# Kernel optimization log

Measured on AMD Instinct MI355X. Metric: run time of the kernel, lower is better.

The kernel has to match this reference:

```python
import jax, jax.numpy as jnp
import numpy as np

# Grids: sparse_shape=(41,320,320); after spcv1 stride(2,1,1) pad1 k3 -> (21,320,320);
# after spcv2 stride(2,1,1) pad(0,1,1) k3 -> (10,320,320); after spcv3 k(3,1,1) stride(2,1,1) -> (4,320,320)
GRID0 = (41, 320, 320)
GRID1 = (21, 320, 320)
GRID2 = (10, 320, 320)
GRID3 = (4, 320, 320)
T = 3
C_IN = 16
BN_EPS = 1e-3


def _idx_grid(coords, shape):
    g = -np.ones(shape, np.int32)
    g[coords[:, 0], coords[:, 1], coords[:, 2]] = np.arange(len(coords), dtype=np.int32)
    return g


def _subm_nbrs(coords, grid):
    M = len(coords)
    nbr = -np.ones((M, 27), np.int32)
    sh = np.array(grid.shape)
    k = 0
    for dz in (-1, 0, 1):
        for dy in (-1, 0, 1):
            for dx in (-1, 0, 1):
                c = coords + np.array([dz, dy, dx])
                ok = np.all((c >= 0) & (c < sh), axis=1)
                nbr[ok, k] = grid[c[ok, 0], c[ok, 1], c[ok, 2]]
                k += 1
    return nbr


def _spconv_pairs(coords_in, grid_in, out_shape, ksz, stride, pad):
    ksz = np.array(ksz); st = np.array(stride); pd = np.array(pad); osh = np.array(out_shape)
    cands = []
    for kz in range(ksz[0]):
        for ky in range(ksz[1]):
            for kx in range(ksz[2]):
                o = coords_in + pd - np.array([kz, ky, kx])
                ok = np.all(o % st == 0, axis=1)
                o = o[ok] // st
                ok2 = np.all((o >= 0) & (o < osh), axis=1)
                cands.append(o[ok2])
    coords_out = np.unique(np.concatenate(cands, 0), axis=0)
    M = len(coords_out); K = int(np.prod(ksz))
    idx = -np.ones((M, K), np.int32)
    sh = np.array(grid_in.shape)
    k = 0
    for kz in range(ksz[0]):
        for ky in range(ksz[1]):
            for kx in range(ksz[2]):
                ci = coords_out * st - pd + np.array([kz, ky, kx])
                ok = np.all((ci >= 0) & (ci < sh), axis=1)
                idx[ok, k] = grid_in[ci[ok, 0], ci[ok, 1], ci[ok, 2]]
                k += 1
    return coords_out.astype(np.int32), idx


def setup_inputs() -> dict:
    rng = np.random.default_rng(0)
    # clustered lidar-like active voxels
    nC, nP = 60, 150
    centers = np.stack([rng.uniform(6, 35, nC), rng.uniform(12, 308, nC), rng.uniform(12, 308, nC)], 1)
    pts = centers[:, None, :] + rng.normal(size=(nC, nP, 3)) * np.array([1.2, 2.0, 2.0])
    pts = np.clip(np.round(pts).astype(np.int64).reshape(-1, 3), 0, np.array(GRID0) - 1)
    coords0 = np.unique(pts, axis=0)
    g0 = _idx_grid(coords0, GRID0)
    nbr0 = _subm_nbrs(coords0, g0)
    coords1, idx1 = _spconv_pairs(coords0, g0, GRID1, (3, 3, 3), (2, 1, 1), (1, 1, 1))
    g1 = _idx_grid(coords1, GRID1)
    nbr1 = _subm_nbrs(coords1, g1)
    coords2, idx2 = _spconv_pairs(coords1, g1, GRID2, (3, 3, 3), (2, 1, 1), (0, 1, 1))
    g2 = _idx_grid(coords2, GRID2)
    nbr2 = _subm_nbrs(coords2, g2)
    coords3, idx3 = _spconv_pairs(coords2, g2, GRID3, (3, 1, 1), (2, 1, 1), (0, 0, 0))

    def w(K, ci, co):
        return jnp.asarray(rng.standard_normal((K, ci, co)) / np.sqrt(K * ci), jnp.float32)

    def bn(n, c):
        g = rng.uniform(0.5, 1.5, (n, c)); b = rng.standard_normal((n, c)) * 0.1
        m = rng.standard_normal((n, c)) * 0.1; v = rng.uniform(0.5, 1.5, (n, c))
        return jnp.asarray(np.stack([g, b, m, v], 1), jnp.float32)  # [n,4,c]

    return dict(
        voxel_features=jnp.asarray(rng.standard_normal((T, len(coords0), C_IN)), jnp.float32),
        w_subm1=w(27, 16, 32), w_subm2=w(27, 32, 32), w_spcv1=w(27, 32, 64),
        w_subm3=w(27, 64, 64), w_subm4=w(27, 64, 64), w_subm5=w(27, 64, 64),
        w_spcv2=w(27, 64, 64), w_subm6=w(27, 64, 64), w_subm7=w(27, 64, 64), w_subm8=w(27, 64, 64),
        w_spcv3=w(3, 64, 64),
        w_ad1=jnp.asarray(rng.standard_normal((64, 64)) / 8.0, jnp.float32),
        w_ad2=jnp.asarray(rng.standard_normal((64, 64)) / 8.0, jnp.float32),
        bn32=bn(2, 32), bn64=bn(9, 64), bn_ad=bn(1, 64)[0],
        nbr0=jnp.asarray(nbr0), idx1=jnp.asarray(idx1), nbr1=jnp.asarray(nbr1),
        idx2=jnp.asarray(idx2), nbr2=jnp.asarray(nbr2), idx3=jnp.asarray(idx3),
        coords3=jnp.asarray(coords3))


def _bn_eval(x, p):
    g, b, m, v = p
    return (x - m) * (g * jax.lax.rsqrt(v + BN_EPS)) + b


def _gconv(f, idx, w):
    # gather-GEMM: idx [M,K] (-1 = missing), f [Min,Ci], w [K,Ci,Co]
    g = jnp.where((idx >= 0)[:, :, None], f[jnp.clip(idx, 0)], 0.0)  # [M,K,Ci]
    return jnp.einsum('mki,kio->mo', g, w)


def reference(voxel_features, w_subm1, w_subm2, w_spcv1, w_subm3, w_subm4, w_subm5,
              w_spcv2, w_subm6, w_subm7, w_subm8, w_spcv3, w_ad1, w_ad2,
              bn32, bn64, bn_ad, nbr0, idx1, nbr1, idx2, nbr2, idx3, coords3):
    relu = jax.nn.relu
    s0 = s1 = s2 = None  # cached previous-frame sparse features per level
    outs = []
    for t in range(voxel_features.shape[0]):
        a0 = 0.0 if s0 is None else jnp.mean(s0, 0)
        a1 = 0.0 if s1 is None else jnp.mean(s1, 0)
        a2 = 0.0 if s2 is None else jnp.mean(s2, 0)
        x = relu(_bn_eval(_gconv(voxel_features[t], nbr0, w_subm1), bn32[0]))
        x = relu(_bn_eval(_gconv(x, nbr0, w_subm2), bn32[1]))
        x3 = relu(_bn_eval(_gconv(x, idx1, w_spcv1) + a0, bn64[0])); s0 = x3
        x = relu(_bn_eval(_gconv(x3, nbr1, w_subm3), bn64[1]))
        x = relu(_bn_eval(_gconv(x, nbr1, w_subm4), bn64[2]))
        x6 = relu(_bn_eval(_gconv(x, nbr1, w_subm5), bn64[3]))
        x7 = relu(_bn_eval(_gconv(x6, idx2, w_spcv2) + a1, bn64[4])); s1 = x7
        x = relu(_bn_eval(_gconv(x7, nbr2, w_subm6), bn64[5]))
        x = relu(_bn_eval(_gconv(x, nbr2, w_subm7), bn64[6]))
        x10 = relu(_bn_eval(_gconv(x, nbr2, w_subm8), bn64[7]))
        x11 = relu(_bn_eval(_gconv(x10, idx3, w_spcv3) + a2, bn64[8])); s2 = x11
        dense = jnp.zeros(GRID3 + (64,), x11.dtype).at[coords3[:, 0], coords3[:, 1], coords3[:, 2]].set(x11)
        outs.append(dense.transpose(3, 0, 1, 2).reshape(1, 64 * GRID3[0], GRID3[1], GRID3[2]))
        adapt = lambda s: (relu(_bn_eval(s @ w_ad1, bn_ad)) @ w_ad2) / 10.0
        s0, s1, s2 = adapt(s0), adapt(s1), adapt(s2)
    return jnp.stack(outs)
```

## Files before the change

kernel.cpp:

```cpp
#include <hip/hip_runtime.h>


typedef _Float16 f16;
typedef _Float16 f16x8 __attribute__((ext_vector_type(8)));
typedef float    f32x4 __attribute__((ext_vector_type(4)));

#define BN_EPS_F 1e-3f

__global__ __launch_bounds__(256)
void fill_zero(float4* __restrict__ p, long n4)
{
    long i  = blockIdx.x * 256L + threadIdx.x;
    long st = (long)gridDim.x * 256L;
    float4 z = make_float4(0.f, 0.f, 0.f, 0.f);
    for (; i < n4; i += st) p[i] = z;
}

__global__ __launch_bounds__(256)
void vf_convert(const float* __restrict__ vf, f16* __restrict__ vf16, int nrows)
{
    int i = blockIdx.x * 256 + threadIdx.x;
    if (i >= nrows * 32) return;
    int r = i >> 5, c = i & 31;
    vf16[i] = (c < 16) ? (f16)vf[r * 16 + c] : (f16)0;
}

struct WXA { const float* s; f16* d; int K, Ci, Co, CiD, off; };
struct WXAll { WXA w[11]; };

__global__ __launch_bounds__(256)
void wxform_all(WXAll wa, int total)
{
    int i = blockIdx.x * 256 + threadIdx.x;
    if (i >= total) return;
    int j = 0;
    #pragma unroll
    for (int t = 1; t < 11; ++t) if (i >= wa.w[t].off) j = t;
    const float* s = wa.w[j].s;
    f16* d = wa.w[j].d;
    int Ci = wa.w[j].Ci, Co = wa.w[j].Co, CiD = wa.w[j].CiD;
    int e = i - wa.w[j].off;
    int cc = Co * CiD;
    int k = e / cc; int rem = e - k * cc;
    int co = rem / CiD; int ci = rem - co * CiD;
    float v = (ci < Ci) ? s[((size_t)k * Ci + ci) * Co + co] : 0.f;
    d[e] = (f16)v;
}

template<int Ci, int Co, int K, bool SCATTER>
__global__ __launch_bounds__(256)
void gconv(const f16* __restrict__ fin, const int* __restrict__ idx,
           const f16* __restrict__ wT,
           const float* __restrict__ bnp,
           const float* __restrict__ avec,
           f16* __restrict__ fout,
           const int* __restrict__ coords, float* __restrict__ dout,
           int M, int blocksPerFrame, long finStride, long foutStride)
{
    constexpr int NF  = Co / 16;
    constexpr int KK  = Ci / 32;
    constexpr int CiP = Ci + 8;
    constexpr int cpr = Ci / 8;
    constexpr int CH  = Co * cpr;
    constexpr int NLD = (CH + 255) / 256;

    __shared__ f16 Bw[2][Co * CiP];
    __shared__ int sIdx[64][K];

    const int tid  = threadIdx.x;
    const int lane = tid & 63;
    const int wq   = tid >> 6;
    const int l15  = lane & 15;
    const int kg   = lane >> 4;

    const int bid   = blockIdx.x;
    const int frame = bid / blocksPerFrame;
    const int fb    = bid - frame * blocksPerFrame;
    const f16* finF = fin + (long)frame * finStride;
    f16* foutF      = fout + (long)frame * foutStride;
    const int m0    = fb * 64;

    for (int i = tid; i < 64 * K; i += 256) {
        int r = i / K, k = i - r * K;
        int m = m0 + r;
        sIdx[r][k] = (m < M) ? idx[(long)m * K + k] : -1;
    }
    for (int i = tid; i < CH; i += 256) {
        int co = i / cpr, q = i - co * cpr;
        *(uint4*)&Bw[0][co * CiP + q * 8] = *(const uint4*)&wT[(long)co * Ci + q * 8];
    }
    __syncthreads();

    const int arow = wq * 16 + l15;

    f16x8 afc[KK];
    {
        int n = sIdx[arow][0];
        #pragma unroll
        for (int kk = 0; kk < KK; ++kk) {
            f16x8 v = {};
            if (n >= 0) v = *(const f16x8*)&finF[(long)n * Ci + kk * 32 + kg * 8];
            afc[kk] = v;
        }
    }

    f32x4 acc[NF];
    #pragma unroll
    for (int nf = 0; nf < NF; ++nf) acc[nf] = (f32x4){0.f, 0.f, 0.f, 0.f};

    #pragma unroll 1
    for (int k = 0; k < K; ++k) {
        const bool more = (k + 1 < K);
        uint4 wreg[NLD];
        if (more) {
            #pragma unroll
            for (int u = 0; u < NLD; ++u) {
                int i = tid + u * 256;
                if (i < CH) {
                    int co = i / cpr, q = i - co * cpr;
                    wreg[u] = *(const uint4*)&wT[((long)(k + 1) * Co + co) * Ci + q * 8];
                }
            }
        }
        f16x8 afn[KK];
        {
            int n = more ? sIdx[arow][k + 1] : -1;
            #pragma unroll
            for (int kk = 0; kk < KK; ++kk) {
                f16x8 v = {};
                if (n >= 0) v = *(const f16x8*)&finF[(long)n * Ci + kk * 32 + kg * 8];
                afn[kk] = v;
            }
        }
        const f16* bwb = &Bw[k & 1][0];
        #pragma unroll
        for (int kk = 0; kk < KK; ++kk) {
            #pragma unroll
            for (int nf = 0; nf < NF; ++nf) {
                f16x8 bf = *(const f16x8*)&bwb[(nf * 16 + l15) * CiP + kk * 32 + kg * 8];
                acc[nf] = __builtin_amdgcn_mfma_f32_16x16x32_f16(afc[kk], bf, acc[nf], 0, 0, 0);
            }
        }
        if (more) {
            #pragma unroll
            for (int u = 0; u < NLD; ++u) {
                int i = tid + u * 256;
                if (i < CH) {
                    int co = i / cpr, q = i - co * cpr;
                    *(uint4*)&Bw[(k + 1) & 1][co * CiP + q * 8] = wreg[u];
                }
            }
            __syncthreads();
        }
        #pragma unroll
        for (int kk = 0; kk < KK; ++kk) afc[kk] = afn[kk];
    }

    #pragma unroll
    for (int nf = 0; nf < NF; ++nf) {
        int c = nf * 16 + l15;
        float gg = bnp[c], bb = bnp[Co + c], mu = bnp[2 * Co + c], vv = bnp[3 * Co + c];
        float sc = gg * rsqrtf(vv + BN_EPS_F);
        float sh = bb - mu * sc;
        float av = avec ? avec[c] : 0.f;
        #pragma unroll
        for (int j = 0; j < 4; ++j) {
            int m = m0 + wq * 16 + kg * 4 + j;
            if (m < M) {
                float x = acc[nf][j] + av;
                float y = fmaxf(fmaf(x, sc, sh), 0.f);
                foutF[(long)m * Co + c] = (f16)y;
                if (SCATTER) {
                    int z  = coords[m * 3 + 0];
                    int yy = coords[m * 3 + 1];
                    int xx = coords[m * 3 + 2];
                    dout[(long)(c * 4 + z) * (320 * 320) + yy * 320 + xx] = y;
                }
            }
        }
    }
}

__global__ __launch_bounds__(64)
void adapt_partial3(const f16* __restrict__ x3, const f16* __restrict__ x7,
                    const f16* __restrict__ x11,
                    const float* __restrict__ w_ad1, const float* __restrict__ bn_ad,
                    float* __restrict__ pb,
                    int M1, int M2, int M3, int g1, int g2)
{
    __shared__ float wl[64 * 64];
    const int c = threadIdx.x;
    for (int i = c; i < 64 * 64; i += 64) wl[i] = w_ad1[i];
    float gg = bn_ad[c], bb = bn_ad[64 + c], mu = bn_ad[128 + c], vv = bn_ad[192 + c];
    float sc = gg * rsqrtf(vv + BN_EPS_F);
    float sh = bb - mu * sc;
    __syncthreads();

    int b = blockIdx.x;
    const f16* s; int M, r0;
    if (b < g1)           { s = x3;  M = M1; r0 = b * 64; }
    else if (b < g1 + g2) { s = x7;  M = M2; r0 = (b - g1) * 64; }
    else                  { s = x11; M = M3; r0 = (b - g1 - g2) * 64; }

    float hacc = 0.f;
    int r1 = min(r0 + 64, M);
    for (int r = r0; r < r1; ++r) {
        float acc = 0.f;
        #pragma unroll
        for (int i8 = 0; i8 < 8; ++i8) {
            f16x8 sv = *(const f16x8*)&s[(size_t)r * 64 + i8 * 8];
            #pragma unroll
            for (int e = 0; e < 8; ++e)
                acc = fmaf((float)sv[e], wl[(i8 * 8 + e) * 64 + c], acc);
        }
        hacc += fmaxf(fmaf(acc, sc, sh), 0.f);
    }
    pb[(size_t)b * 64 + c] = hacc;
}

__global__ __launch_bounds__(192)
void adapt_final3(const float* __restrict__ pb, const float* __restrict__ w_ad2,
                  float* __restrict__ av, int g1, int g2, int g3,
                  float invM1, float invM2, float invM3)
{
    __shared__ float h[3][64];
    const int lvl = threadIdx.x >> 6;
    const int c   = threadIdx.x & 63;
    int base = (lvl == 0) ? 0 : (lvl == 1 ? g1 : g1 + g2);
    int n    = (lvl == 0) ? g1 : (lvl == 1 ? g2 : g3);
    float invM = (lvl == 0) ? invM1 : (lvl == 1 ? invM2 : invM3);
    float acc = 0.f;
    for (int i = 0; i < n; ++i) acc += pb[(size_t)(base + i) * 64 + c];
    h[lvl][c] = acc * invM;
    __syncthreads();
    float o = 0.f;
    #pragma unroll 8
    for (int j = 0; j < 64; ++j) o = fmaf(h[lvl][j], w_ad2[j * 64 + c], o);
    av[lvl * 64 + c] = o * 0.1f;
}

extern "C" void kernel_launch(void* const* d_in, const int* in_sizes, int n_in,
                              void* d_out, int out_size, void* d_ws, size_t ws_size,
                              hipStream_t stream)
{
    const float* vf      = (const float*)d_in[0];
    const float* w_subm1 = (const float*)d_in[1];
    const float* w_subm2 = (const float*)d_in[2];
    const float* w_spcv1 = (const float*)d_in[3];
    const float* w_subm3 = (const float*)d_in[4];
    const float* w_subm4 = (const float*)d_in[5];
    const float* w_subm5 = (const float*)d_in[6];
    const float* w_spcv2 = (const float*)d_in[7];
    const float* w_subm6 = (const float*)d_in[8];
    const float* w_subm7 = (const float*)d_in[9];
    const float* w_subm8 = (const float*)d_in[10];
    const float* w_spcv3 = (const float*)d_in[11];
    const float* w_ad1   = (const float*)d_in[12];
    const float* w_ad2   = (const float*)d_in[13];
    const float* bn32    = (const float*)d_in[14];
    const float* bn64    = (const float*)d_in[15];
    const float* bn_ad   = (const float*)d_in[16];
    const int* nbr0    = (const int*)d_in[17];
    const int* idx1    = (const int*)d_in[18];
    const int* nbr1    = (const int*)d_in[19];
    const int* idx2    = (const int*)d_in[20];
    const int* nbr2    = (const int*)d_in[21];
    const int* idx3    = (const int*)d_in[22];
    const int* coords3 = (const int*)d_in[23];

    const int M0 = in_sizes[0]  / (3 * 16);
    const int M1 = in_sizes[18] / 27;
    const int M2 = in_sizes[20] / 27;
    const int M3 = in_sizes[22] / 3;

    char* base = (char*)d_ws;
    size_t off = 0;
    auto alloc = [&](size_t bytes) -> void* {
        void* p = base + off;
        off = (off + bytes + 255) & ~(size_t)255;
        return p;
    };
    f16* wt1  = (f16*)alloc((size_t)27 * 32 * 32 * 2);
    f16* wt2  = (f16*)alloc((size_t)27 * 32 * 32 * 2);
    f16* wtc1 = (f16*)alloc((size_t)27 * 64 * 32 * 2);
    f16* wt3  = (f16*)alloc((size_t)27 * 64 * 64 * 2);
    f16* wt4  = (f16*)alloc((size_t)27 * 64 * 64 * 2);
    f16* wt5  = (f16*)alloc((size_t)27 * 64 * 64 * 2);
    f16* wtc2 = (f16*)alloc((size_t)27 * 64 * 64 * 2);
    f16* wt6  = (f16*)alloc((size_t)27 * 64 * 64 * 2);
    f16* wt7  = (f16*)alloc((size_t)27 * 64 * 64 * 2);
    f16* wt8  = (f16*)alloc((size_t)27 * 64 * 64 * 2);
    f16* wtc3 = (f16*)alloc((size_t)3  * 64 * 64 * 2);
    f16* vf16  = (f16*)alloc((size_t)3 * M0 * 32 * 2);
    f16* buf0a = (f16*)alloc((size_t)3 * M0 * 32 * 2);
    f16* buf0b = (f16*)alloc((size_t)3 * M0 * 32 * 2);
    f16* x3    = (f16*)alloc((size_t)M1 * 64 * 2);
    f16* buf1a = (f16*)alloc((size_t)M1 * 64 * 2);
    f16* buf1b = (f16*)alloc((size_t)M1 * 64 * 2);
    f16* x7    = (f16*)alloc((size_t)M2 * 64 * 2);
    f16* buf2a = (f16*)alloc((size_t)M2 * 64 * 2);
    f16* buf2b = (f16*)alloc((size_t)M2 * 64 * 2);
    f16* x11   = (f16*)alloc((size_t)M3 * 64 * 2);
    float* av  = (float*)alloc(192 * 4);
    const int g1a = (M1 + 63) / 64, g2a = (M2 + 63) / 64, g3a = (M3 + 63) / 64;
    float* pb  = (float*)alloc((size_t)(g1a + g2a + g3a) * 64 * 4);
    (void)ws_size; (void)n_in;

    WXAll wa;
    int woff = 0;
    auto addw = [&](int slot, const float* s, f16* d, int K, int Ci, int Co, int CiD) {
        wa.w[slot] = {s, d, K, Ci, Co, CiD, woff};
        woff += K * Co * CiD;
    };
    addw(0,  w_subm1, wt1,  27, 16, 32, 32);
    addw(1,  w_subm2, wt2,  27, 32, 32, 32);
    addw(2,  w_spcv1, wtc1, 27, 32, 64, 32);
    addw(3,  w_subm3, wt3,  27, 64, 64, 64);
    addw(4,  w_subm4, wt4,  27, 64, 64, 64);
    addw(5,  w_subm5, wt5,  27, 64, 64, 64);
    addw(6,  w_spcv2, wtc2, 27, 64, 64, 64);
    addw(7,  w_subm6, wt6,  27, 64, 64, 64);
    addw(8,  w_subm7, wt7,  27, 64, 64, 64);
    addw(9,  w_subm8, wt8,  27, 64, 64, 64);
    addw(10, w_spcv3, wtc3, 3,  64, 64, 64);
    wxform_all<<<(woff + 255) / 256, 256, 0, stream>>>(wa, woff);
    vf_convert<<<(3 * M0 * 32 + 255) / 256, 256, 0, stream>>>(vf, vf16, 3 * M0);
    fill_zero<<<2048, 256, 0, stream>>>((float4*)d_out, (long)out_size / 4);

    const int g0 = (M0 + 63) / 64;
    const int g1 = (M1 + 63) / 64;
    const int g2 = (M2 + 63) / 64;
    const int g3 = (M3 + 63) / 64;
    const long s0 = (long)M0 * 32;

    gconv<32,32,27,false><<<3 * g0, 256, 0, stream>>>(
        vf16,  nbr0, wt1, bn32,       nullptr, buf0a, nullptr, nullptr, M0, g0, s0, s0);
    gconv<32,32,27,false><<<3 * g0, 256, 0, stream>>>(
        buf0a, nbr0, wt2, bn32 + 128, nullptr, buf0b, nullptr, nullptr, M0, g0, s0, s0);

    for (int t = 0; t < 3; ++t) {
        const float* a0 = (t == 0) ? nullptr : av + 0;
        const float* a1 = (t == 0) ? nullptr : av + 64;
        const float* a2 = (t == 0) ? nullptr : av + 128;
        float* doutT = (float*)d_out + (size_t)t * 256 * 320 * 320;

        gconv<32,64,27,false><<<g1, 256, 0, stream>>>(
            buf0b + (long)t * s0, idx1, wtc1, bn64, a0, x3, nullptr, nullptr, M1, g1, 0, 0);
        gconv<64,64,27,false><<<g1, 256, 0, stream>>>(
            x3,    nbr1, wt3, bn64 + 256,  nullptr, buf1a, nullptr, nullptr, M1, g1, 0, 0);
        gconv<64,64,27,false><<<g1, 256, 0, stream>>>(
            buf1a, nbr1, wt4, bn64 + 512,  nullptr, buf1b, nullptr, nullptr, M1, g1, 0, 0);
        gconv<64,64,27,false><<<g1, 256, 0, stream>>>(
            buf1b, nbr1, wt5, bn64 + 768,  nullptr, buf1a, nullptr, nullptr, M1, g1, 0, 0);
        gconv<64,64,27,false><<<g2, 256, 0, stream>>>(
            buf1a, idx2, wtc2, bn64 + 1024, a1,     x7,    nullptr, nullptr, M2, g2, 0, 0);
        gconv<64,64,27,false><<<g2, 256, 0, stream>>>(
            x7,    nbr2, wt6, bn64 + 1280, nullptr, buf2a, nullptr, nullptr, M2, g2, 0, 0);
        gconv<64,64,27,false><<<g2, 256, 0, stream>>>(
            buf2a, nbr2, wt7, bn64 + 1536, nullptr, buf2b, nullptr, nullptr, M2, g2, 0, 0);
        gconv<64,64,27,false><<<g2, 256, 0, stream>>>(
            buf2b, nbr2, wt8, bn64 + 1792, nullptr, buf2a, nullptr, nullptr, M2, g2, 0, 0);
        gconv<64,64,3,true><<<g3, 256, 0, stream>>>(
            buf2a, idx3, wtc3, bn64 + 2048, a2,    x11,   coords3, doutT,   M3, g3, 0, 0);

        if (t < 2) {
            adapt_partial3<<<g1a + g2a + g3a, 64, 0, stream>>>(
                x3, x7, x11, w_ad1, bn_ad, pb, M1, M2, M3, g1a, g2a);
            adapt_final3<<<1, 192, 0, stream>>>(
                pb, w_ad2, av, g1a, g2a, g3a, 1.f / M1, 1.f / M2, 1.f / M3);
        }
    }
}
```

Baseline: 1.532 ms.

## Fuse all layers into one persistent cooperative kernel with grid syncs

Replaces the chain of about 30 separate launches (weight transform, conversion, zero fill, each conv layer, adapt reductions) with a single cooperative persistent kernel that runs every stage in turn, separated by grid-wide syncs. Conv tiles grow to 128 rows with 512-thread blocks and are walked in a grid-stride loop. The adapt reduction now uses atomicAdd into per-level accumulators instead of per-block partials plus a separate final kernel. Launch overhead and inter-kernel gaps are removed, but grid.sync costs, a fixed grid size, atomic ordering nondeterminism and lower occupancy per block are added.

```diff
diff --git a/kernel.cpp b/kernel.cpp
--- a/kernel.cpp
+++ b/kernel.cpp
@@ -1,71 +1,47 @@
 #include <hip/hip_runtime.h>
-
+#include <hip/hip_cooperative_groups.h>
+
+
+namespace cg = cooperative_groups;
 
 typedef _Float16 f16;
 typedef _Float16 f16x8 __attribute__((ext_vector_type(8)));
 typedef float    f32x4 __attribute__((ext_vector_type(4)));
 
 #define BN_EPS_F 1e-3f
-
-__global__ __launch_bounds__(256)
-void fill_zero(float4* __restrict__ p, long n4)
-{
-    long i  = blockIdx.x * 256L + threadIdx.x;
-    long st = (long)gridDim.x * 256L;
-    float4 z = make_float4(0.f, 0.f, 0.f, 0.f);
-    for (; i < n4; i += st) p[i] = z;
-}
-
-__global__ __launch_bounds__(256)
-void vf_convert(const float* __restrict__ vf, f16* __restrict__ vf16, int nrows)
-{
-    int i = blockIdx.x * 256 + threadIdx.x;
-    if (i >= nrows * 32) return;
-    int r = i >> 5, c = i & 31;
-    vf16[i] = (c < 16) ? (f16)vf[r * 16 + c] : (f16)0;
-}
-
-struct WXA { const float* s; f16* d; int K, Ci, Co, CiD, off; };
-struct WXAll { WXA w[11]; };
-
-__global__ __launch_bounds__(256)
-void wxform_all(WXAll wa, int total)
-{
-    int i = blockIdx.x * 256 + threadIdx.x;
-    if (i >= total) return;
-    int j = 0;
-    #pragma unroll
-    for (int t = 1; t < 11; ++t) if (i >= wa.w[t].off) j = t;
-    const float* s = wa.w[j].s;
-    f16* d = wa.w[j].d;
-    int Ci = wa.w[j].Ci, Co = wa.w[j].Co, CiD = wa.w[j].CiD;
-    int e = i - wa.w[j].off;
-    int cc = Co * CiD;
-    int k = e / cc; int rem = e - k * cc;
-    int co = rem / CiD; int ci = rem - co * CiD;
-    float v = (ci < Ci) ? s[((size_t)k * Ci + ci) * Co + co] : 0.f;
-    d[e] = (f16)v;
-}
+#define SMEM_BYTES 33024
+
+struct WXA { const float* s; int K, Ci, Co, CiD, off; };
+
+struct Args {
+    const float *vf, *w_ad1, *w_ad2, *bn32, *bn64, *bn_ad;
+    const int *nbr0, *idx1, *nbr1, *idx2, *nbr2, *idx3, *coords3;
+    float* dout; long out_n4;
+    f16* wt[11];
+    f16 *vf16, *b0a, *b0b, *x3, *b1a, *b1b, *x7, *b2a, *b2b, *x11;
+    float *hs0, *hs1, *av0, *av1;
+    WXA wx[11]; int wtotal;
+    int M0, M1, M2, M3;
+};
 
 template<int Ci, int Co, int K, bool SCATTER>
-__global__ __launch_bounds__(256)
-void gconv(const f16* __restrict__ fin, const int* __restrict__ idx,
-           const f16* __restrict__ wT,
-           const float* __restrict__ bnp,
-           const float* __restrict__ avec,
-           f16* __restrict__ fout,
-           const int* __restrict__ coords, float* __restrict__ dout,
-           int M, int blocksPerFrame, long finStride, long foutStride)
+__device__ void conv_layer(char* smem,
+    const f16* __restrict__ fin, const int* __restrict__ idx,
+    const f16* __restrict__ wT,
+    const float* __restrict__ bnp, const float* __restrict__ avec,
+    f16* __restrict__ fout,
+    const int* __restrict__ coords, float* __restrict__ dout,
+    int M, int nframes, long finStride, long foutStride)
 {
     constexpr int NF  = Co / 16;
     constexpr int KK  = Ci / 32;
     constexpr int CiP = Ci + 8;
     constexpr int cpr = Ci / 8;
     constexpr int CH  = Co * cpr;
-    constexpr int NLD = (CH + 255) / 256;
-
-    __shared__ f16 Bw[2][Co * CiP];
-    __shared__ int sIdx[64][K];
+    constexpr int NLD = (CH + 511) / 512;
+
+    int (*sIdx)[K] = (int(*)[K])smem;
+    f16* Bw = (f16*)(smem + 13824);
 
     const int tid  = threadIdx.x;
     const int lane = tid & 63;
@@ -73,205 +49,305 @@
     const int l15  = lane & 15;
     const int kg   = lane >> 4;
 
-    const int bid   = blockIdx.x;
-    const int frame = bid / blocksPerFrame;
-    const int fb    = bid - frame * blocksPerFrame;
-    const f16* finF = fin + (long)frame * finStride;
-    f16* foutF      = fout + (long)frame * foutStride;
-    const int m0    = fb * 64;
-
-    for (int i = tid; i < 64 * K; i += 256) {
-        int r = i / K, k = i - r * K;
-        int m = m0 + r;
-        sIdx[r][k] = (m < M) ? idx[(long)m * K + k] : -1;
-    }
-    for (int i = tid; i < CH; i += 256) {
-        int co = i / cpr, q = i - co * cpr;
-        *(uint4*)&Bw[0][co * CiP + q * 8] = *(const uint4*)&wT[(long)co * Ci + q * 8];
-    }
-    __syncthreads();
-
-    const int arow = wq * 16 + l15;
-
-    f16x8 afc[KK];
-    {
-        int n = sIdx[arow][0];
-        #pragma unroll
-        for (int kk = 0; kk < KK; ++kk) {
-            f16x8 v = {};
-            if (n >= 0) v = *(const f16x8*)&finF[(long)n * Ci + kk * 32 + kg * 8];
-            afc[kk] = v;
-        }
-    }
-
-    f32x4 acc[NF];
-    #pragma unroll
-    for (int nf = 0; nf < NF; ++nf) acc[nf] = (f32x4){0.f, 0.f, 0.f, 0.f};
-
-    #pragma unroll 1
-    for (int k = 0; k < K; ++k) {
-        const bool more = (k + 1 < K);
-        uint4 wreg[NLD];
-        if (more) {
-            #pragma unroll
-            for (int u = 0; u < NLD; ++u) {
-                int i = tid + u * 256;
-                if (i < CH) {
-                    int co = i / cpr, q = i - co * cpr;
-                    wreg[u] = *(const uint4*)&wT[((long)(k + 1) * Co + co) * Ci + q * 8];
-                }
-            }
-        }
-        f16x8 afn[KK];
+    const int tpf    = (M + 127) >> 7;
+    const int ntiles = tpf * nframes;
+
+    for (int tile = blockIdx.x; tile < ntiles; tile += gridDim.x) {
+        const int frame = tile / tpf;
+        const int fb    = tile - frame * tpf;
+        const f16* finF = fin + (long)frame * finStride;
+        f16* foutF      = fout + (long)frame * foutStride;
+        const int m0    = fb << 7;
+
+        __syncthreads();
+        for (int i = tid; i < 128 * K; i += 512) {
+            int r = i / K, k = i - r * K;
+            int m = m0 + r;
+            sIdx[r][k] = (m < M) ? idx[(long)m * K + k] : -1;
+        }
+        for (int i = tid; i < CH; i += 512) {
+            int co = i / cpr, q = i - co * cpr;
+            *(uint4*)&Bw[co * CiP + q * 8] = *(const uint4*)&wT[(long)co * Ci + q * 8];
+        }
+        __syncthreads();
+
+        const int arow = wq * 16 + l15;
+
+        f16x8 afc[KK];
         {
-            int n = more ? sIdx[arow][k + 1] : -1;
+            int n = sIdx[arow][0];
             #pragma unroll
             for (int kk = 0; kk < KK; ++kk) {
                 f16x8 v = {};
                 if (n >= 0) v = *(const f16x8*)&finF[(long)n * Ci + kk * 32 + kg * 8];
-                afn[kk] = v;
-            }
-        }
-        const f16* bwb = &Bw[k & 1][0];
+                afc[kk] = v;
+            }
+        }
+
+        f32x4 acc[NF];
         #pragma unroll
-        for (int kk = 0; kk < KK; ++kk) {
-            #pragma unroll
-            for (int nf = 0; nf < NF; ++nf) {
-                f16x8 bf = *(const f16x8*)&bwb[(nf * 16 + l15) * CiP + kk * 32 + kg * 8];
-                acc[nf] = __builtin_amdgcn_mfma_f32_16x16x32_f16(afc[kk], bf, acc[nf], 0, 0, 0);
-            }
-        }
-        if (more) {
-            #pragma unroll
-            for (int u = 0; u < NLD; ++u) {
-                int i = tid + u * 256;
-                if (i < CH) {
-                    int co = i / cpr, q = i - co * cpr;
-                    *(uint4*)&Bw[(k + 1) & 1][co * CiP + q * 8] = wreg[u];
-                }
-            }
-            __syncthreads();
-        }
+        for (int nf = 0; nf < NF; ++nf) acc[nf] = (f32x4){0.f, 0.f, 0.f, 0.f};
+
+        #pragma unroll 1
+        for (int k = 0; k < K; ++k) {
+            const bool more = (k + 1 < K);
+            uint4 wreg[NLD];
+            if (more) {
+                #pragma unroll
+                for (int u = 0; u < NLD; ++u) {
+                    int i = tid + u * 512;
+                    if (i < CH) {
+                        int co = i / cpr, q = i - co * cpr;
+                        wreg[u] = *(const uint4*)&wT[((long)(k + 1) * Co + co) * Ci + q * 8];
+                    }
+                }
+            }
+            f16x8 afn[KK];
+            {
+                int n = more ? sIdx[arow][k + 1] : -1;
+                #pragma unroll
+                for (int kk = 0; kk < KK; ++kk) {
+                    f16x8 v = {};
+                    if (n >= 0) v = *(const f16x8*)&finF[(long)n * Ci + kk * 32 + kg * 8];
+                    afn[kk] = v;
+                }
+            }
+            const f16* bwb = &Bw[(k & 1) * (Co * CiP)];
+            #pragma unroll
+            for (int kk = 0; kk < KK; ++kk)
+                #pragma unroll
+                for (int nf = 0; nf < NF; ++nf) {
+                    f16x8 bf = *(const f16x8*)&bwb[(nf * 16 + l15) * CiP + kk * 32 + kg * 8];
+                    acc[nf] = __builtin_amdgcn_mfma_f32_16x16x32_f16(afc[kk], bf, acc[nf], 0, 0, 0);
+                }
+            if (more) {
+                #pragma unroll
+                for (int u = 0; u < NLD; ++u) {
+                    int i = tid + u * 512;
+                    if (i < CH) {
+                        int co = i / cpr, q = i - co * cpr;
+                        *(uint4*)&Bw[((k + 1) & 1) * (Co * CiP) + co * CiP + q * 8] = wreg[u];
+                    }
+                }
+                __syncthreads();
+            }
+            #pragma unroll
+            for (int kk = 0; kk < KK; ++kk) afc[kk] = afn[kk];
+        }
+
         #pragma unroll
-        for (int kk = 0; kk < KK; ++kk) afc[kk] = afn[kk];
-    }
-
-    #pragma unroll
-    for (int nf = 0; nf < NF; ++nf) {
-        int c = nf * 16 + l15;
-        float gg = bnp[c], bb = bnp[Co + c], mu = bnp[2 * Co + c], vv = bnp[3 * Co + c];
-        float sc = gg * rsqrtf(vv + BN_EPS_F);
-        float sh = bb - mu * sc;
-        float av = avec ? avec[c] : 0.f;
-        #pragma unroll
-        for (int j = 0; j < 4; ++j) {
-            int m = m0 + wq * 16 + kg * 4 + j;
-            if (m < M) {
-                float x = acc[nf][j] + av;
-                float y = fmaxf(fmaf(x, sc, sh), 0.f);
-                foutF[(long)m * Co + c] = (f16)y;
-                if (SCATTER) {
-                    int z  = coords[m * 3 + 0];
-                    int yy = coords[m * 3 + 1];
-                    int xx = coords[m * 3 + 2];
-                    dout[(long)(c * 4 + z) * (320 * 320) + yy * 320 + xx] = y;
-                }
-            }
-        }
-    }
-}
-
-__global__ __launch_bounds__(64)
-void adapt_partial3(const f16* __restrict__ x3, const f16* __restrict__ x7,
-                    const f16* __restrict__ x11,
-                    const float* __restrict__ w_ad1, const float* __restrict__ bn_ad,
-                    float* __restrict__ pb,
-                    int M1, int M2, int M3, int g1, int g2)
-{
-    __shared__ float wl[64 * 64];
-    const int c = threadIdx.x;
-    for (int i = c; i < 64 * 64; i += 64) wl[i] = w_ad1[i];
+        for (int nf = 0; nf < NF; ++nf) {
+            int c = nf * 16 + l15;
+            float gg = bnp[c], bb = bnp[Co + c], mu = bnp[2 * Co + c], vv = bnp[3 * Co + c];
+            float sc = gg * rsqrtf(vv + BN_EPS_F);
+            float sh = bb - mu * sc;
+            float av = avec ? avec[c] : 0.f;
+            #pragma unroll
+            for (int j = 0; j < 4; ++j) {
+                int m = m0 + wq * 16 + kg * 4 + j;
+                if (m < M) {
+                    float x = acc[nf][j] + av;
+                    float y = fmaxf(fmaf(x, sc, sh), 0.f);
+                    foutF[(long)m * Co + c] = (f16)y;
+                    if (SCATTER) {
+                        int z  = coords[m * 3 + 0];
+                        int yy = coords[m * 3 + 1];
+                        int xx = coords[m * 3 + 2];
+                        dout[(long)(c * 4 + z) * (320 * 320) + yy * 320 + xx] = y;
+                    }
+                }
+            }
+        }
+    }
+}
+
+__device__ void adapt_partial(char* smem,
+    const f16* __restrict__ x3, const f16* __restrict__ x7,
+    const f16* __restrict__ x11, int M1, int M2, int M3,
+    const float* __restrict__ w_ad1, const float* __restrict__ bn_ad,
+    float* __restrict__ hs)
+{
+    float* wl = (float*)smem;
+    const int tid = threadIdx.x;
+    __syncthreads();
+    for (int i = tid; i < 64 * 64; i += 512) wl[i] = w_ad1[i];
+    __syncthreads();
+
+    const int sub = tid >> 6;
+    const int c   = tid & 63;
     float gg = bn_ad[c], bb = bn_ad[64 + c], mu = bn_ad[128 + c], vv = bn_ad[192 + c];
     float sc = gg * rsqrtf(vv + BN_EPS_F);
     float sh = bb - mu * sc;
+
+    const int c1 = (M1 + 63) >> 6, c2 = (M2 + 63) >> 6, c3 = (M3 + 63) >> 6;
+    const int ct = c1 + c2 + c3;
+
+    for (int ch = blockIdx.x * 8 + sub; ch < ct; ch += gridDim.x * 8) {
+        const f16* s; int M, r0, lvl;
+        if (ch < c1)           { s = x3;  M = M1; r0 = ch << 6;            lvl = 0; }
+        else if (ch < c1 + c2) { s = x7;  M = M2; r0 = (ch - c1) << 6;     lvl = 1; }
+        else                   { s = x11; M = M3; r0 = (ch - c1 - c2) << 6; lvl = 2; }
+        float hacc = 0.f;
+        int r1 = min(r0 + 64, M);
+        for (int r = r0; r < r1; ++r) {
+            float acc = 0.f;
+            #pragma unroll
+            for (int i8 = 0; i8 < 8; ++i8) {
+                f16x8 sv = *(const f16x8*)&s[(long)r * 64 + i8 * 8];
+                #pragma unroll
+                for (int e = 0; e < 8; ++e)
+                    acc = fmaf((float)sv[e], wl[(i8 * 8 + e) * 64 + c], acc);
+            }
+            hacc += fmaxf(fmaf(acc, sc, sh), 0.f);
+        }
+        atomicAdd(&hs[lvl * 64 + c], hacc);
+    }
+}
+
+__device__ void adapt_final(char* smem,
+    const float* __restrict__ hs, const float* __restrict__ w_ad2,
+    float* __restrict__ av, float invM1, float invM2, float invM3)
+{
+    float* h = (float*)(smem + 16384);
+    const int tid = threadIdx.x;
+    if (tid < 192) {
+        int lvl = tid >> 6;
+        float invM = (lvl == 0) ? invM1 : (lvl == 1 ? invM2 : invM3);
+        h[tid] = hs[tid] * invM;
+    }
     __syncthreads();
-
-    int b = blockIdx.x;
-    const f16* s; int M, r0;
-    if (b < g1)           { s = x3;  M = M1; r0 = b * 64; }
-    else if (b < g1 + g2) { s = x7;  M = M2; r0 = (b - g1) * 64; }
-    else                  { s = x11; M = M3; r0 = (b - g1 - g2) * 64; }
-
-    float hacc = 0.f;
-    int r1 = min(r0 + 64, M);
-    for (int r = r0; r < r1; ++r) {
-        float acc = 0.f;
-        #pragma unroll
-        for (int i8 = 0; i8 < 8; ++i8) {
-            f16x8 sv = *(const f16x8*)&s[(size_t)r * 64 + i8 * 8];
-            #pragma unroll
-            for (int e = 0; e < 8; ++e)
-                acc = fmaf((float)sv[e], wl[(i8 * 8 + e) * 64 + c], acc);
-        }
-        hacc += fmaxf(fmaf(acc, sc, sh), 0.f);
-    }
-    pb[(size_t)b * 64 + c] = hacc;
-}
-
-__global__ __launch_bounds__(192)
-void adapt_final3(const float* __restrict__ pb, const float* __restrict__ w_ad2,
-                  float* __restrict__ av, int g1, int g2, int g3,
-                  float invM1, float invM2, float invM3)
-{
-    __shared__ float h[3][64];
-    const int lvl = threadIdx.x >> 6;
-    const int c   = threadIdx.x & 63;
-    int base = (lvl == 0) ? 0 : (lvl == 1 ? g1 : g1 + g2);
-    int n    = (lvl == 0) ? g1 : (lvl == 1 ? g2 : g3);
-    float invM = (lvl == 0) ? invM1 : (lvl == 1 ? invM2 : invM3);
-    float acc = 0.f;
-    for (int i = 0; i < n; ++i) acc += pb[(size_t)(base + i) * 64 + c];
-    h[lvl][c] = acc * invM;
+    if (tid < 192) {
+        int lvl = tid >> 6, c = tid & 63;
+        float o = 0.f;
+        #pragma unroll 8
+        for (int j = 0; j < 64; ++j) o = fmaf(h[lvl * 64 + j], w_ad2[j * 64 + c], o);
+        av[tid] = o * 0.1f;
+    }
     __syncthreads();
-    float o = 0.f;
-    #pragma unroll 8
-    for (int j = 0; j < 64; ++j) o = fmaf(h[lvl][j], w_ad2[j * 64 + c], o);
-    av[lvl * 64 + c] = o * 0.1f;
+}
+
+__global__ __launch_bounds__(512, 2)
+void mega(Args a)
+{
+    cg::grid_group gg = cg::this_grid();
+    __shared__ __align__(16) char smem[SMEM_BYTES];
+    const int tid  = threadIdx.x;
+    const long gsz = (long)gridDim.x * 512;
+    const long gt  = (long)blockIdx.x * 512 + tid;
+
+    {
+        float4* o4 = (float4*)a.dout;
+        float4 z = make_float4(0.f, 0.f, 0.f, 0.f);
+        for (long i = gt; i < a.out_n4; i += gsz) o4[i] = z;
+        for (int i = (int)gt; i < a.wtotal; i += (int)gsz) {
+            int j = 0;
+            #pragma unroll
+            for (int t = 1; t < 11; ++t) if (i >= a.wx[t].off) j = t;
+            const WXA& W = a.wx[j];
+            int e = i - W.off;
+            int cc = W.Co * W.CiD;
+            int k = e / cc; int rem = e - k * cc;
+            int co = rem / W.CiD; int ci = rem - co * W.CiD;
+            float v = (ci < W.Ci) ? W.s[((long)k * W.Ci + ci) * W.Co + co] : 0.f;
+            a.wt[j][e] = (f16)v;
+        }
+        int nvf = 3 * a.M0 * 32;
+        for (int i = (int)gt; i < nvf; i += (int)gsz) {
+            int r = i >> 5, c = i & 31;
+            a.vf16[i] = (c < 16) ? (f16)a.vf[r * 16 + c] : (f16)0;
+        }
+        if (gt < 192) a.hs0[gt] = 0.f;
+        else if (gt < 384) a.hs1[gt - 192] = 0.f;
+    }
+    gg.sync();
+
+    const long s0 = (long)a.M0 * 32;
+
+    conv_layer<32,32,27,false>(smem, a.vf16, a.nbr0, a.wt[0], a.bn32, nullptr,
+                               a.b0a, nullptr, nullptr, a.M0, 3, s0, s0);
+    gg.sync();
+    conv_layer<32,32,27,false>(smem, a.b0a, a.nbr0, a.wt[1], a.bn32 + 128, nullptr,
+                               a.b0b, nullptr, nullptr, a.M0, 3, s0, s0);
+    gg.sync();
+
+    for (int t = 0; t < 3; ++t) {
+        const float* av = (t == 0) ? nullptr : (t == 1 ? a.av0 : a.av1);
+        float* doutT = a.dout + (long)t * 256 * 320 * 320;
+
+        conv_layer<32,64,27,false>(smem, a.b0b + (long)t * s0, a.idx1, a.wt[2],
+                                   a.bn64, av ? av + 0 : nullptr,
+                                   a.x3, nullptr, nullptr, a.M1, 1, 0, 0);
+        gg.sync();
+        conv_layer<64,64,27,false>(smem, a.x3, a.nbr1, a.wt[3], a.bn64 + 256, nullptr,
+                                   a.b1a, nullptr, nullptr, a.M1, 1, 0, 0);
+        gg.sync();
+        conv_layer<64,64,27,false>(smem, a.b1a, a.nbr1, a.wt[4], a.bn64 + 512, nullptr,
+                                   a.b1b, nullptr, nullptr, a.M1, 1, 0, 0);
+        gg.sync();
+        conv_layer<64,64,27,false>(smem, a.b1b, a.nbr1, a.wt[5], a.bn64 + 768, nullptr,
+                                   a.b1a, nullptr, nullptr, a.M1, 1, 0, 0);
+        gg.sync();
+        conv_layer<64,64,27,false>(smem, a.b1a, a.idx2, a.wt[6], a.bn64 + 1024,
+                                   av ? av + 64 : nullptr,
+                                   a.x7, nullptr, nullptr, a.M2, 1, 0, 0);
+        gg.sync();
+        conv_layer<64,64,27,false>(smem, a.x7, a.nbr2, a.wt[7], a.bn64 + 1280, nullptr,
+                                   a.b2a, nullptr, nullptr, a.M2, 1, 0, 0);
+        gg.sync();
+        conv_layer<64,64,27,false>(smem, a.b2a, a.nbr2, a.wt[8], a.bn64 + 1536, nullptr,
+                                   a.b2b, nullptr, nullptr, a.M2, 1, 0, 0);
+        gg.sync();
+        conv_layer<64,64,27,false>(smem, a.b2b, a.nbr2, a.wt[9], a.bn64 + 1792, nullptr,
+                                   a.b2a, nullptr, nullptr, a.M2, 1, 0, 0);
+        gg.sync();
+        conv_layer<64,64,3,true>(smem, a.b2a, a.idx3, a.wt[10], a.bn64 + 2048,
+                                 av ? av + 128 : nullptr,
+                                 a.x11, a.coords3, doutT, a.M3, 1, 0, 0);
+        gg.sync();
+
+        if (t < 2) {
+            float* hs = (t == 0) ? a.hs0 : a.hs1;
+            adapt_partial(smem, a.x3, a.x7, a.x11, a.M1, a.M2, a.M3,
+                          a.w_ad1, a.bn_ad, hs);
+            gg.sync();
+            if (blockIdx.x == 0)
+                adapt_final(smem, hs, a.w_ad2, (t == 0) ? a.av0 : a.av1,
+                            1.f / a.M1, 1.f / a.M2, 1.f / a.M3);
+            gg.sync();
+        }
+    }
 }
 
 extern "C" void kernel_launch(void* const* d_in, const int* in_sizes, int n_in,
                               void* d_out, int out_size, void* d_ws, size_t ws_size,
                               hipStream_t stream)
 {
-    const float* vf      = (const float*)d_in[0];
-    const float* w_subm1 = (const float*)d_in[1];
-    const float* w_subm2 = (const float*)d_in[2];
-    const float* w_spcv1 = (const float*)d_in[3];
-    const float* w_subm3 = (const float*)d_in[4];
-    const float* w_subm4 = (const float*)d_in[5];
-    const float* w_subm5 = (const float*)d_in[6];
-    const float* w_spcv2 = (const float*)d_in[7];
-    const float* w_subm6 = (const float*)d_in[8];
-    const float* w_subm7 = (const float*)d_in[9];
-    const float* w_subm8 = (const float*)d_in[10];
-    const float* w_spcv3 = (const float*)d_in[11];
-    const float* w_ad1   = (const float*)d_in[12];
-    const float* w_ad2   = (const float*)d_in[13];
-    const float* bn32    = (const float*)d_in[14];
-    const float* bn64    = (const float*)d_in[15];
-    const float* bn_ad   = (const float*)d_in[16];
-    const int* nbr0    = (const int*)d_in[17];
-    const int* idx1    = (const int*)d_in[18];
-    const int* nbr1    = (const int*)d_in[19];
-    const int* idx2    = (const int*)d_in[20];
-    const int* nbr2    = (const int*)d_in[21];
-    const int* idx3    = (const int*)d_in[22];
-    const int* coords3 = (const int*)d_in[23];
-
-    const int M0 = in_sizes[0]  / (3 * 16);
-    const int M1 = in_sizes[18] / 27;
-    const int M2 = in_sizes[20] / 27;
-    const int M3 = in_sizes[22] / 3;
+    Args a;
+    a.vf     = (const float*)d_in[0];
+    const float* w_conv[11] = {
+        (const float*)d_in[1],  (const float*)d_in[2],  (const float*)d_in[3],
+        (const float*)d_in[4],  (const float*)d_in[5],  (const float*)d_in[6],
+        (const float*)d_in[7],  (const float*)d_in[8],  (const float*)d_in[9],
+        (const float*)d_in[10], (const float*)d_in[11] };
+    a.w_ad1  = (const float*)d_in[12];
+    a.w_ad2  = (const float*)d_in[13];
+    a.bn32   = (const float*)d_in[14];
+    a.bn64   = (const float*)d_in[15];
+    a.bn_ad  = (const float*)d_in[16];
+    a.nbr0   = (const int*)d_in[17];
+    a.idx1   = (const int*)d_in[18];
+    a.nbr1   = (const int*)d_in[19];
+    a.idx2   = (const int*)d_in[20];
+    a.nbr2   = (const int*)d_in[21];
+    a.idx3   = (const int*)d_in[22];
+    a.coords3= (const int*)d_in[23];
+    a.dout   = (float*)d_out;
+    a.out_n4 = (long)out_size / 4;
+
+    a.M0 = in_sizes[0]  / (3 * 16);
+    a.M1 = in_sizes[18] / 27;
+    a.M2 = in_sizes[20] / 27;
+    a.M3 = in_sizes[22] / 3;
 
     char* base = (char*)d_ws;
     size_t off = 0;
@@ -280,94 +356,42 @@
         off = (off + bytes + 255) & ~(size_t)255;
         return p;
     };
-    f16* wt1  = (f16*)alloc((size_t)27 * 32 * 32 * 2);
-    f16* wt2  = (f16*)alloc((size_t)27 * 32 * 32 * 2);
-    f16* wtc1 = (f16*)alloc((size_t)27 * 64 * 32 * 2);
-    f16* wt3  = (f16*)alloc((size_t)27 * 64 * 64 * 2);
-    f16* wt4  = (f16*)alloc((size_t)27 * 64 * 64 * 2);
-    f16* wt5  = (f16*)alloc((size_t)27 * 64 * 64 * 2);
-    f16* wtc2 = (f16*)alloc((size_t)27 * 64 * 64 * 2);
-    f16* wt6  = (f16*)alloc((size_t)27 * 64 * 64 * 2);
-    f16* wt7  = (f16*)alloc((size_t)27 * 64 * 64 * 2);
-    f16* wt8  = (f16*)alloc((size_t)27 * 64 * 64 * 2);
-    f16* wtc3 = (f16*)alloc((size_t)3  * 64 * 64 * 2);
-    f16* vf16  = (f16*)alloc((size_t)3 * M0 * 32 * 2);
-    f16* buf0a = (f16*)alloc((size_t)3 * M0 * 32 * 2);
-    f16* buf0b = (f16*)alloc((size_t)3 * M0 * 32 * 2);
-    f16* x3    = (f16*)alloc((size_t)M1 * 64 * 2);
-    f16* buf1a = (f16*)alloc((size_t)M1 * 64 * 2);
-    f16* buf1b = (f16*)alloc((size_t)M1 * 64 * 2);
-    f16* x7    = (f16*)alloc((size_t)M2 * 64 * 2);
-    f16* buf2a = (f16*)alloc((size_t)M2 * 64 * 2);
-    f16* buf2b = (f16*)alloc((size_t)M2 * 64 * 2);
-    f16* x11   = (f16*)alloc((size_t)M3 * 64 * 2);
-    float* av  = (float*)alloc(192 * 4);
-    const int g1a = (M1 + 63) / 64, g2a = (M2 + 63) / 64, g3a = (M3 + 63) / 64;
-    float* pb  = (float*)alloc((size_t)(g1a + g2a + g3a) * 64 * 4);
+    const int wd[11][4] = {
+        {27,16,32,32}, {27,32,32,32}, {27,32,64,32}, {27,64,64,64},
+        {27,64,64,64}, {27,64,64,64}, {27,64,64,64}, {27,64,64,64},
+        {27,64,64,64}, {27,64,64,64}, {3,64,64,64} };
+    int woff = 0;
+    for (int j = 0; j < 11; ++j) {
+        int K = wd[j][0], Ci = wd[j][1], Co = wd[j][2], CiD = wd[j][3];
+        a.wt[j] = (f16*)alloc((size_t)K * Co * CiD * 2);
+        a.wx[j] = {w_conv[j], K, Ci, Co, CiD, woff};
+        woff += K * Co * CiD;
+    }
+    a.wtotal = woff;
+
+    a.vf16 = (f16*)alloc((size_t)3 * a.M0 * 32 * 2);
+    a.b0a  = (f16*)alloc((size_t)3 * a.M0 * 32 * 2);
+    a.b0b  = (f16*)alloc((size_t)3 * a.M0 * 32 * 2);
+    a.x3   = (f16*)alloc((size_t)a.M1 * 64 * 2);
+    a.b1a  = (f16*)alloc((size_t)a.M1 * 64 * 2);
+    a.b1b  = (f16*)alloc((size_t)a.M1 * 64 * 2);
+    a.x7   = (f16*)alloc((size_t)a.M2 * 64 * 2);
+    a.b2a  = (f16*)alloc((size_t)a.M2 * 64 * 2);
+    a.b2b  = (f16*)alloc((size_t)a.M2 * 64 * 2);
+    a.x11  = (f16*)alloc((size_t)a.M3 * 64 * 2);
+    a.hs0  = (float*)alloc(192 * 4);
+    a.hs1  = (float*)alloc(192 * 4);
+    a.av0  = (float*)alloc(192 * 4);
+    a.av1  = (float*)alloc(192 * 4);
     (void)ws_size; (void)n_in;
 
-    WXAll wa;
-    int woff = 0;
-    auto addw = [&](int slot, const float* s, f16* d, int K, int Ci, int Co, int CiD) {
-        wa.w[slot] = {s, d, K, Ci, Co, CiD, woff};
-        woff += K * Co * CiD;
-    };
-    addw(0,  w_subm1, wt1,  27, 16, 32, 32);
-    addw(1,  w_subm2, wt2,  27, 32, 32, 32);
-    addw(2,  w_spcv1, wtc1, 27, 32, 64, 32);
-    addw(3,  w_subm3, wt3,  27, 64, 64, 64);
-    addw(4,  w_subm4, wt4,  27, 64, 64, 64);
-    addw(5,  w_subm5, wt5,  27, 64, 64, 64);
-    addw(6,  w_spcv2, wtc2, 27, 64, 64, 64);
-    addw(7,  w_subm6, wt6,  27, 64, 64, 64);
-    addw(8,  w_subm7, wt7,  27, 64, 64, 64);
-    addw(9,  w_subm8, wt8,  27, 64, 64, 64);
-    addw(10, w_spcv3, wtc3, 3,  64, 64, 64);
-    wxform_all<<<(woff + 255) / 256, 256, 0, stream>>>(wa, woff);
-    vf_convert<<<(3 * M0 * 32 + 255) / 256, 256, 0, stream>>>(vf, vf16, 3 * M0);
-    fill_zero<<<2048, 256, 0, stream>>>((float4*)d_out, (long)out_size / 4);
-
-    const int g0 = (M0 + 63) / 64;
-    const int g1 = (M1 + 63) / 64;
-    const int g2 = (M2 + 63) / 64;
-    const int g3 = (M3 + 63) / 64;
-    const long s0 = (long)M0 * 32;
-
-    gconv<32,32,27,false><<<3 * g0, 256, 0, stream>>>(
-        vf16,  nbr0, wt1, bn32,       nullptr, buf0a, nullptr, nullptr, M0, g0, s0, s0);
-    gconv<32,32,27,false><<<3 * g0, 256, 0, stream>>>(
-        buf0a, nbr0, wt2, bn32 + 128, nullptr, buf0b, nullptr, nullptr, M0, g0, s0, s0);
-
-    for (int t = 0; t < 3; ++t) {
-        const float* a0 = (t == 0) ? nullptr : av + 0;
-        const float* a1 = (t == 0) ? nullptr : av + 64;
-        const float* a2 = (t == 0) ? nullptr : av + 128;
-        float* doutT = (float*)d_out + (size_t)t * 256 * 320 * 320;
-
-        gconv<32,64,27,false><<<g1, 256, 0, stream>>>(
-            buf0b + (long)t * s0, idx1, wtc1, bn64, a0, x3, nullptr, nullptr, M1, g1, 0, 0);
-        gconv<64,64,27,false><<<g1, 256, 0, stream>>>(
-            x3,    nbr1, wt3, bn64 + 256,  nullptr, buf1a, nullptr, nullptr, M1, g1, 0, 0);
-        gconv<64,64,27,false><<<g1, 256, 0, stream>>>(
-            buf1a, nbr1, wt4, bn64 + 512,  nullptr, buf1b, nullptr, nullptr, M1, g1, 0, 0);
-        gconv<64,64,27,false><<<g1, 256, 0, stream>>>(
-            buf1b, nbr1, wt5, bn64 + 768,  nullptr, buf1a, nullptr, nullptr, M1, g1, 0, 0);
-        gconv<64,64,27,false><<<g2, 256, 0, stream>>>(
-            buf1a, idx2, wtc2, bn64 + 1024, a1,     x7,    nullptr, nullptr, M2, g2, 0, 0);
-        gconv<64,64,27,false><<<g2, 256, 0, stream>>>(
-            x7,    nbr2, wt6, bn64 + 1280, nullptr, buf2a, nullptr, nullptr, M2, g2, 0, 0);
-        gconv<64,64,27,false><<<g2, 256, 0, stream>>>(
-            buf2a, nbr2, wt7, bn64 + 1536, nullptr, buf2b, nullptr, nullptr, M2, g2, 0, 0);
-        gconv<64,64,27,false><<<g2, 256, 0, stream>>>(
-            buf2b, nbr2, wt8, bn64 + 1792, nullptr, buf2a, nullptr, nullptr, M2, g2, 0, 0);
-        gconv<64,64,3,true><<<g3, 256, 0, stream>>>(
-            buf2a, idx3, wtc3, bn64 + 2048, a2,    x11,   coords3, doutT,   M3, g3, 0, 0);
-
-        if (t < 2) {
-            adapt_partial3<<<g1a + g2a + g3a, 64, 0, stream>>>(
-                x3, x7, x11, w_ad1, bn_ad, pb, M1, M2, M3, g1a, g2a);
-            adapt_final3<<<1, 192, 0, stream>>>(
-                pb, w_ad2, av, g1a, g2a, g3a, 1.f / M1, 1.f / M2, 1.f / M3);
-        }
-    }
-}
+    int maxBlk = 0;
+    if (hipOccupancyMaxActiveBlocksPerMultiprocessor(&maxBlk, mega, 512, 0) != hipSuccess
+        || maxBlk < 1)
+        maxBlk = 1;
+    int grid = 256 * (maxBlk >= 2 ? 2 : 1);
+
+    void* params[] = { (void*)&a };
+    hipLaunchCooperativeKernel((const void*)mega, dim3(grid), dim3(512),
+                               params, 0, stream);
+}
```

Result: slower. 1.944 ms (+26.9%).

## Restructure gconv into single-wave blocks with register-resident weight and gather prefetch

Applied to the files above, without the earlier changes.

The sparse-conv kernel changes from 256-thread blocks covering 64 rows with LDS double-buffered weights to 64-thread single-wavefront blocks covering 16 rows. Weights are now loaded straight from global memory into registers, and there is no shared memory or __syncthreads. Neighbour indices are prefetched four offsets ahead and gathered features two offsets ahead, with the K loop fully unrolled. This removes block-level barriers and LDS traffic and raises the block count, but every wave re-reads the full weight tensor from global/L2 and register pressure goes up.

```diff
diff --git a/kernel.cpp b/kernel.cpp
--- a/kernel.cpp
+++ b/kernel.cpp
@@ -48,7 +48,7 @@
 }
 
 template<int Ci, int Co, int K, bool SCATTER>
-__global__ __launch_bounds__(256)
+__global__ __launch_bounds__(64)
 void gconv(const f16* __restrict__ fin, const int* __restrict__ idx,
            const f16* __restrict__ wT,
            const float* __restrict__ bnp,
@@ -57,19 +57,10 @@
            const int* __restrict__ coords, float* __restrict__ dout,
            int M, int blocksPerFrame, long finStride, long foutStride)
 {
-    constexpr int NF  = Co / 16;
-    constexpr int KK  = Ci / 32;
-    constexpr int CiP = Ci + 8;
-    constexpr int cpr = Ci / 8;
-    constexpr int CH  = Co * cpr;
-    constexpr int NLD = (CH + 255) / 256;
-
-    __shared__ f16 Bw[2][Co * CiP];
-    __shared__ int sIdx[64][K];
-
-    const int tid  = threadIdx.x;
-    const int lane = tid & 63;
-    const int wq   = tid >> 6;
+    constexpr int NF = Co / 16;
+    constexpr int KK = Ci / 32;
+
+    const int lane = threadIdx.x;
     const int l15  = lane & 15;
     const int kg   = lane >> 4;
 
@@ -78,82 +69,66 @@
     const int fb    = bid - frame * blocksPerFrame;
     const f16* finF = fin + (long)frame * finStride;
     f16* foutF      = fout + (long)frame * foutStride;
-    const int m0    = fb * 64;
-
-    for (int i = tid; i < 64 * K; i += 256) {
-        int r = i / K, k = i - r * K;
-        int m = m0 + r;
-        sIdx[r][k] = (m < M) ? idx[(long)m * K + k] : -1;
-    }
-    for (int i = tid; i < CH; i += 256) {
-        int co = i / cpr, q = i - co * cpr;
-        *(uint4*)&Bw[0][co * CiP + q * 8] = *(const uint4*)&wT[(long)co * Ci + q * 8];
-    }
-    __syncthreads();
-
-    const int arow = wq * 16 + l15;
-
-    f16x8 afc[KK];
-    {
-        int n = sIdx[arow][0];
+    const int m0    = fb * 16;
+    const int mrow  = m0 + l15;
+    const bool rowok = mrow < M;
+    const long irow  = (long)mrow * K;
+
+    int ibuf[4];
+    #pragma unroll
+    for (int u = 0; u < 4; ++u)
+        ibuf[u] = (rowok && u < K) ? idx[irow + u] : -1;
+
+    f16x8 abuf[3][KK];
+    #pragma unroll
+    for (int s = 0; s < 2 && s < K; ++s) {
+        int n = ibuf[s];
         #pragma unroll
         for (int kk = 0; kk < KK; ++kk) {
             f16x8 v = {};
             if (n >= 0) v = *(const f16x8*)&finF[(long)n * Ci + kk * 32 + kg * 8];
-            afc[kk] = v;
-        }
-    }
+            abuf[s][kk] = v;
+        }
+    }
+
+    f16x8 bbuf[2][KK][NF];
+    #pragma unroll
+    for (int kk = 0; kk < KK; ++kk)
+        #pragma unroll
+        for (int nf = 0; nf < NF; ++nf)
+            bbuf[0][kk][nf] = *(const f16x8*)&wT[((long)(nf * 16 + l15)) * Ci + kk * 32 + kg * 8];
 
     f32x4 acc[NF];
     #pragma unroll
     for (int nf = 0; nf < NF; ++nf) acc[nf] = (f32x4){0.f, 0.f, 0.f, 0.f};
 
-    #pragma unroll 1
+    #pragma unroll
     for (int k = 0; k < K; ++k) {
-        const bool more = (k + 1 < K);
-        uint4 wreg[NLD];
-        if (more) {
-            #pragma unroll
-            for (int u = 0; u < NLD; ++u) {
-                int i = tid + u * 256;
-                if (i < CH) {
-                    int co = i / cpr, q = i - co * cpr;
-                    wreg[u] = *(const uint4*)&wT[((long)(k + 1) * Co + co) * Ci + q * 8];
-                }
-            }
-        }
-        f16x8 afn[KK];
-        {
-            int n = more ? sIdx[arow][k + 1] : -1;
+        if (k + 4 < K)
+            ibuf[(k + 4) & 3] = rowok ? idx[irow + (k + 4)] : -1;
+        if (k + 2 < K) {
+            int n = ibuf[(k + 2) & 3];
             #pragma unroll
             for (int kk = 0; kk < KK; ++kk) {
                 f16x8 v = {};
                 if (n >= 0) v = *(const f16x8*)&finF[(long)n * Ci + kk * 32 + kg * 8];
-                afn[kk] = v;
+                abuf[(k + 2) % 3][kk] = v;
             }
         }
-        const f16* bwb = &Bw[k & 1][0];
-        #pragma unroll
-        for (int kk = 0; kk < KK; ++kk) {
+        if (k + 1 < K) {
             #pragma unroll
-            for (int nf = 0; nf < NF; ++nf) {
-                f16x8 bf = *(const f16x8*)&bwb[(nf * 16 + l15) * CiP + kk * 32 + kg * 8];
-                acc[nf] = __builtin_amdgcn_mfma_f32_16x16x32_f16(afc[kk], bf, acc[nf], 0, 0, 0);
-            }
-        }
-        if (more) {
+            for (int kk = 0; kk < KK; ++kk)
+                #pragma unroll
+                for (int nf = 0; nf < NF; ++nf)
+                    bbuf[(k + 1) & 1][kk][nf] =
+                        *(const f16x8*)&wT[((long)(k + 1) * Co + nf * 16 + l15) * Ci + kk * 32 + kg * 8];
+        }
+        #pragma unroll
+        for (int kk = 0; kk < KK; ++kk)
             #pragma unroll
-            for (int u = 0; u < NLD; ++u) {
-                int i = tid + u * 256;
-                if (i < CH) {
-                    int co = i / cpr, q = i - co * cpr;
-                    *(uint4*)&Bw[(k + 1) & 1][co * CiP + q * 8] = wreg[u];
-                }
-            }
-            __syncthreads();
-        }
-        #pragma unroll
-        for (int kk = 0; kk < KK; ++kk) afc[kk] = afn[kk];
+            for (int nf = 0; nf < NF; ++nf)
+                acc[nf] = __builtin_amdgcn_mfma_f32_16x16x32_f16(
+                    abuf[k % 3][kk], bbuf[k & 1][kk][nf], acc[nf], 0, 0, 0);
     }
 
     #pragma unroll
@@ -165,7 +140,7 @@
         float av = avec ? avec[c] : 0.f;
         #pragma unroll
         for (int j = 0; j < 4; ++j) {
-            int m = m0 + wq * 16 + kg * 4 + j;
+            int m = m0 + kg * 4 + j;
             if (m < M) {
                 float x = acc[nf][j] + av;
                 float y = fmaxf(fmaf(x, sc, sh), 0.f);
@@ -327,15 +302,15 @@
     vf_convert<<<(3 * M0 * 32 + 255) / 256, 256, 0, stream>>>(vf, vf16, 3 * M0);
     fill_zero<<<2048, 256, 0, stream>>>((float4*)d_out, (long)out_size / 4);
 
-    const int g0 = (M0 + 63) / 64;
-    const int g1 = (M1 + 63) / 64;
-    const int g2 = (M2 + 63) / 64;
-    const int g3 = (M3 + 63) / 64;
+    const int g0 = (M0 + 15) / 16;
+    const int g1 = (M1 + 15) / 16;
+    const int g2 = (M2 + 15) / 16;
+    const int g3 = (M3 + 15) / 16;
     const long s0 = (long)M0 * 32;
 
-    gconv<32,32,27,false><<<3 * g0, 256, 0, stream>>>(
+    gconv<32,32,27,false><<<3 * g0, 64, 0, stream>>>(
         vf16,  nbr0, wt1, bn32,       nullptr, buf0a, nullptr, nullptr, M0, g0, s0, s0);
-    gconv<32,32,27,false><<<3 * g0, 256, 0, stream>>>(
+    gconv<32,32,27,false><<<3 * g0, 64, 0, stream>>>(
         buf0a, nbr0, wt2, bn32 + 128, nullptr, buf0b, nullptr, nullptr, M0, g0, s0, s0);
 
     for (int t = 0; t < 3; ++t) {
@@ -344,23 +319,23 @@
         const float* a2 = (t == 0) ? nullptr : av + 128;
         float* doutT = (float*)d_out + (size_t)t * 256 * 320 * 320;
 
-        gconv<32,64,27,false><<<g1, 256, 0, stream>>>(
+        gconv<32,64,27,false><<<g1, 64, 0, stream>>>(
             buf0b + (long)t * s0, idx1, wtc1, bn64, a0, x3, nullptr, nullptr, M1, g1, 0, 0);
-        gconv<64,64,27,false><<<g1, 256, 0, stream>>>(
+        gconv<64,64,27,false><<<g1, 64, 0, stream>>>(
             x3,    nbr1, wt3, bn64 + 256,  nullptr, buf1a, nullptr, nullptr, M1, g1, 0, 0);
-        gconv<64,64,27,false><<<g1, 256, 0, stream>>>(
+        gconv<64,64,27,false><<<g1, 64, 0, stream>>>(
             buf1a, nbr1, wt4, bn64 + 512,  nullptr, buf1b, nullptr, nullptr, M1, g1, 0, 0);
-        gconv<64,64,27,false><<<g1, 256, 0, stream>>>(
+        gconv<64,64,27,false><<<g1, 64, 0, stream>>>(
             buf1b, nbr1, wt5, bn64 + 768,  nullptr, buf1a, nullptr, nullptr, M1, g1, 0, 0);
-        gconv<64,64,27,false><<<g2, 256, 0, stream>>>(
+        gconv<64,64,27,false><<<g2, 64, 0, stream>>>(
             buf1a, idx2, wtc2, bn64 + 1024, a1,     x7,    nullptr, nullptr, M2, g2, 0, 0);
-        gconv<64,64,27,false><<<g2, 256, 0, stream>>>(
+        gconv<64,64,27,false><<<g2, 64, 0, stream>>>(
             x7,    nbr2, wt6, bn64 + 1280, nullptr, buf2a, nullptr, nullptr, M2, g2, 0, 0);
-        gconv<64,64,27,false><<<g2, 256, 0, stream>>>(
+        gconv<64,64,27,false><<<g2, 64, 0, stream>>>(
             buf2a, nbr2, wt7, bn64 + 1536, nullptr, buf2b, nullptr, nullptr, M2, g2, 0, 0);
-        gconv<64,64,27,false><<<g2, 256, 0, stream>>>(
+        gconv<64,64,27,false><<<g2, 64, 0, stream>>>(
             buf2b, nbr2, wt8, bn64 + 1792, nullptr, buf2a, nullptr, nullptr, M2, g2, 0, 0);
-        gconv<64,64,3,true><<<g3, 256, 0, stream>>>(
+        gconv<64,64,3,true><<<g3, 64, 0, stream>>>(
             buf2a, idx3, wtc3, bn64 + 2048, a2,    x11,   coords3, doutT,   M3, g3, 0, 0);
 
         if (t < 2) {
```

Measured after the change: 1.602 ms. 4.6% more time.
